# Kernel tuning notes

Measured on AMD Instinct MI355X. Metric: run time of the kernel, lower is better.

The kernel has to match this reference:

```python
import jax, jax.numpy as jnp
import numpy as np

N, D, H, DEG = 20000, 128, 128, 32


def setup_inputs() -> dict:
    key = jax.random.key(0)
    ks = jax.random.split(key, 6)
    s = 0.02
    h = jax.random.normal(ks[0], (N, D), dtype=jnp.float32)
    # per-node neighbor indices, sorted by index (permutation invariance per docstring)
    nbr_idx = jnp.sort(jax.random.randint(ks[1], (N, DEG), 0, N), axis=-1)
    W_ih = jax.random.normal(ks[2], (4 * H, D), dtype=jnp.float32) * s
    W_hh = jax.random.normal(ks[3], (4 * H, H), dtype=jnp.float32) * s
    b_ih = jnp.zeros((4 * H,), jnp.float32)
    b_hh = jnp.zeros((4 * H,), jnp.float32)
    W_out = jax.random.normal(ks[4], (H, D + H), dtype=jnp.float32) * s
    b_out = jnp.zeros((H,), jnp.float32)
    return {"h": h, "nbr_idx": nbr_idx, "W_ih": W_ih, "W_hh": W_hh,
            "b_ih": b_ih, "b_hh": b_hh, "W_out": W_out, "b_out": b_out}


def reference(h, nbr_idx, W_ih, W_hh, b_ih, b_hh, W_out, b_out):
    # Gather neighbor features: [N, DEG, D]
    nbr = h[nbr_idx]
    # Precompute input-to-gate projections for all steps: [N, DEG, 4H]
    xg = jnp.einsum('ndi,gi->ndg', nbr, W_ih) + b_ih + b_hh
    xg = jnp.swapaxes(xg, 0, 1)  # [DEG, N, 4H] for scan over neighbor sequence
    h0 = jnp.zeros((h.shape[0], W_hh.shape[1]), h.dtype)
    c0 = jnp.zeros_like(h0)

    def step(carry, g_t):
        hp, cp = carry
        g = g_t + hp @ W_hh.T            # [N, 4H]
        i, f, gg, o = jnp.split(g, 4, axis=-1)  # PyTorch gate order i,f,g,o
        c = jax.nn.sigmoid(f) * cp + jax.nn.sigmoid(i) * jnp.tanh(gg)
        hn = jax.nn.sigmoid(o) * jnp.tanh(c)
        return (hn, c), None

    (agg, _), _ = jax.lax.scan(step, (h0, c0), xg)  # agg = final hidden state [N, H]
    combined = jnp.concatenate([h, agg], axis=-1)   # [N, D+H]
    return jax.nn.relu(combined @ W_out.T + b_out)  # [N, H]
```

## Files before the change

kernel.cpp:

```cpp
#include <hip/hip_runtime.h>

#define NN 20000
#define DD 128
#define HH 128
#define G4 512
#define DEG 32
#define NPB 32
#define PAIRS 625
#define GRID2 512

typedef __attribute__((ext_vector_type(4))) float f32x4;
typedef __attribute__((ext_vector_type(8))) short s16x8;

#ifndef __has_builtin
#define __has_builtin(x) 0
#endif

__device__ int g_cnt;

static __device__ __forceinline__ float fexp2(float x){
#if __has_builtin(__builtin_amdgcn_exp2f)
  return __builtin_amdgcn_exp2f(x);
#else
  return exp2f(x);
#endif
}
static __device__ __forceinline__ float frcp(float x){
#if __has_builtin(__builtin_amdgcn_rcpf)
  return __builtin_amdgcn_rcpf(x);
#else
  return 1.f/x;
#endif
}

static __device__ __forceinline__ unsigned cvt_pk_bf16(float lo, float hi){
  unsigned r;
  asm("v_cvt_pk_bf16_f32 %0, %1, %2" : "=v"(r) : "v"(lo), "v"(hi));
  return r;
}
static __device__ __forceinline__ s16x8 ld8bf(const float* __restrict__ p){
  f32x4 a = *(const f32x4*)p;
  f32x4 b = *(const f32x4*)(p+4);
  union{unsigned u[4]; s16x8 v;} z;
  z.u[0]=cvt_pk_bf16(a[0],a[1]);
  z.u[1]=cvt_pk_bf16(a[2],a[3]);
  z.u[2]=cvt_pk_bf16(b[0],b[1]);
  z.u[3]=cvt_pk_bf16(b[2],b[3]);
  return z.v;
}
static __device__ __forceinline__ s16x8 ld8bf_s(const float* __restrict__ p, float s){
  f32x4 a = *(const f32x4*)p;
  f32x4 b = *(const f32x4*)(p+4);
  union{unsigned u[4]; s16x8 v;} z;
  z.u[0]=cvt_pk_bf16(a[0]*s,a[1]*s);
  z.u[1]=cvt_pk_bf16(a[2]*s,a[3]*s);
  z.u[2]=cvt_pk_bf16(b[0]*s,b[1]*s);
  z.u[3]=cvt_pk_bf16(b[2]*s,b[3]*s);
  return z.v;
}
static __device__ __forceinline__ float lo16f(unsigned u){
  union{unsigned x; float f;} v; v.x = u << 16; return v.f;
}
static __device__ __forceinline__ float hi16f(unsigned u){
  union{unsigned x; float f;} v; v.x = u & 0xffff0000u; return v.f;
}
#define NLOG2E -1.44269504f
#define TLOG2E  2.88539008f

__global__ __launch_bounds__(512,2) void k_hp(
    const float* __restrict__ h, const float* __restrict__ W_ih,
    const float* __restrict__ b_ih, const float* __restrict__ b_hh,
    unsigned short* __restrict__ Hp)
{
  if(blockIdx.x==0 && threadIdx.x==0) g_cnt = GRID2;
  const int tid=threadIdx.x, w=tid>>6, lane=tid&63, lo=lane&15, hi=lane>>4;
  const float SC[4]={NLOG2E,NLOG2E,TLOG2E,NLOG2E};
  s16x8 A[4][4];
#pragma unroll
  for(int g=0;g<4;++g){
    const float* wr=W_ih+(size_t)(128*g+16*w+lo)*DD+8*hi;
#pragma unroll
    for(int c=0;c<4;++c) A[g][c]=ld8bf_s(wr+32*c, SC[g]);
  }
  f32x4 bb[4];
#pragma unroll
  for(int g=0;g<4;++g){
    const int gcb=128*g+16*w+4*hi;
    bb[g]=(*(const f32x4*)(b_ih+gcb) + *(const f32x4*)(b_hh+gcb))*SC[g];
  }
  const int nchunk = (blockIdx.x < 57) ? 2 : 1;
  for(int cc=0; cc<nchunk; ++cc){
    const int n0 = ((cc? 256+blockIdx.x : blockIdx.x))*64;
    f32x4 acc[4][4];
#pragma unroll
    for(int g=0;g<4;++g)
#pragma unroll
      for(int nt=0;nt<4;++nt) acc[g][nt]=(f32x4)0.f;
#pragma unroll
    for(int c=0;c<4;++c){
      s16x8 B[4];
#pragma unroll
      for(int nt=0;nt<4;++nt){
        int nd=n0+16*nt+lo; if(nd>=NN) nd=NN-1;
        B[nt]=ld8bf(h+(size_t)nd*DD+32*c+8*hi);
      }
#pragma unroll
      for(int g=0;g<4;++g)
#pragma unroll
        for(int nt=0;nt<4;++nt)
          acc[g][nt]=__builtin_amdgcn_mfma_f32_16x16x32_bf16(A[g][c],B[nt],acc[g][nt],0,0,0);
    }
#pragma unroll
    for(int nt=0;nt<4;++nt){
      int nd=n0+16*nt+lo;
      if(nd<NN){
        unsigned short* p = Hp + (size_t)nd*G4 + w*64 + hi*16;
        uint4 q0, q1;
        q0.x=cvt_pk_bf16(acc[0][nt][0]+bb[0][0], acc[0][nt][1]+bb[0][1]);
        q0.y=cvt_pk_bf16(acc[0][nt][2]+bb[0][2], acc[0][nt][3]+bb[0][3]);
        q0.z=cvt_pk_bf16(acc[1][nt][0]+bb[1][0], acc[1][nt][1]+bb[1][1]);
        q0.w=cvt_pk_bf16(acc[1][nt][2]+bb[1][2], acc[1][nt][3]+bb[1][3]);
        q1.x=cvt_pk_bf16(acc[2][nt][0]+bb[2][0], acc[2][nt][1]+bb[2][1]);
        q1.y=cvt_pk_bf16(acc[2][nt][2]+bb[2][2], acc[2][nt][3]+bb[2][3]);
        q1.z=cvt_pk_bf16(acc[3][nt][0]+bb[3][0], acc[3][nt][1]+bb[3][1]);
        q1.w=cvt_pk_bf16(acc[3][nt][2]+bb[3][2], acc[3][nt][3]+bb[3][3]);
        *(uint4*)p = q0;
        *(uint4*)(p+8) = q1;
      }
    }
  }
}

static __device__ __forceinline__ void unpack_acc(const uint4 q[2], f32x4 acc[4]){
  acc[0][0]=lo16f(q[0].x); acc[0][1]=hi16f(q[0].x); acc[0][2]=lo16f(q[0].y); acc[0][3]=hi16f(q[0].y);
  acc[1][0]=lo16f(q[0].z); acc[1][1]=hi16f(q[0].z); acc[1][2]=lo16f(q[0].w); acc[1][3]=hi16f(q[0].w);
  acc[2][0]=lo16f(q[1].x); acc[2][1]=hi16f(q[1].x); acc[2][2]=lo16f(q[1].y); acc[2][3]=hi16f(q[1].y);
  acc[3][0]=lo16f(q[1].z); acc[3][1]=hi16f(q[1].z); acc[3][2]=lo16f(q[1].w); acc[3][3]=hi16f(q[1].w);
}

static __device__ __forceinline__ void cell_update(const f32x4 acc[4], float C[4],
                                                   char* wb, int waddr){
  float hv[4];
#pragma unroll
  for(int r=0;r<4;++r){
    float ei=fexp2(acc[0][r]);
    float ef=fexp2(acc[1][r]);
    float eg=fexp2(acc[2][r]);
    float eo=fexp2(acc[3][r]);
    float itgT=__builtin_fmaf(eg, TLOG2E, -TLOG2E)*frcp((1.f+ei)*(1.f+eg));
    float Cn=__builtin_fmaf(C[r], frcp(1.f+ef), itgT);
    C[r]=Cn;
    float ec=fexp2(Cn);
    hv[r]=(ec-1.f)*frcp((1.f+eo)*(1.f+ec));
  }
  uint2 pk;
  pk.x=cvt_pk_bf16(hv[0],hv[1]);
  pk.y=cvt_pk_bf16(hv[2],hv[3]);
  *(uint2*)(wb + waddr) = pk;
}

__global__ __launch_bounds__(512,2) void k_lstm(
    const float* __restrict__ h, const int* __restrict__ nbr,
    const float* __restrict__ W_hh, const unsigned short* __restrict__ Hp,
    const float* __restrict__ W_out, const float* __restrict__ b_out,
    float* __restrict__ out)
{
  __shared__ unsigned short hpA[16*HH];
  __shared__ unsigned short hpB[16*HH];
  __shared__ int nlds[DEG*NPB];
  __shared__ int spair;
  const int tid=threadIdx.x, w=tid>>6, lane=tid&63, lo=lane&15, hi=lane>>4;
  const int swz=(lo&7)<<4;
  const int woff=w*64+hi*16;
  const int waddr=((lo*256 + 32*w + 8*hi) ^ swz);
  const float SC[4]={NLOG2E,NLOG2E,TLOG2E,NLOG2E};

  s16x8 A[4][4];
#pragma unroll
  for(int g=0;g<4;++g){
    const float* wr=W_hh+(size_t)(128*g+16*w+lo)*HH+8*hi;
#pragma unroll
    for(int c=0;c<4;++c) A[g][c]=ld8bf_s(wr+32*c, SC[g]);
  }

  int pair = blockIdx.x;
  for(;;){
    const int n0 = pair*NPB;
    {
      unsigned* za=(unsigned*)&hpA[0];
      unsigned* zb=(unsigned*)&hpB[0];
      za[tid]=0u; za[tid+512]=0u;
      zb[tid]=0u; zb[tid+512]=0u;
#pragma unroll
      for(int i=0;i<2;++i){
        int idx=tid+512*i;
        nlds[(idx&31)*NPB + (idx>>5)] = nbr[n0*DEG + idx]*G4;
      }
    }
    __syncthreads();

    float cstA[4]={0.f,0.f,0.f,0.f}, cstB[4]={0.f,0.f,0.f,0.f};
    f32x4 accA[4], accB[4];
#pragma unroll
    for(int g=0;g<4;++g) accB[g]=(f32x4)0.f;

    uint4 qAx[2], qAy[2], qBx[2], qBy[2];
    {
      const unsigned short* ga=Hp+(size_t)nlds[lo]+woff;
      const unsigned short* gb=Hp+(size_t)nlds[16+lo]+woff;
      qAx[0]=*(const uint4*)ga; qAx[1]=*(const uint4*)(ga+8);
      qBx[0]=*(const uint4*)gb; qBx[1]=*(const uint4*)(gb+8);
    }

#define INTERVAL_P(QUSE, QLOAD, TLOAD) { \
      { const unsigned short* gp_=Hp+(size_t)nlds[(TLOAD)*NPB+lo]+woff; \
        QLOAD[0]=*(const uint4*)gp_; QLOAD[1]=*(const uint4*)(gp_+8); } \
      s16x8 Ba[4]; \
      const char* ra=(const char*)&hpA[0]; \
      _Pragma("unroll") \
      for(int c=0;c<4;++c) Ba[c]=*(const s16x8*)(ra + (((lo*256 + 64*c + 16*hi)) ^ swz)); \
      cell_update(accB, cstB, (char*)&hpB[0], waddr); \
      unpack_acc(QUSE, accA); \
      _Pragma("unroll") \
      for(int c=0;c<4;++c) \
        _Pragma("unroll") \
        for(int g=0;g<4;++g) \
          accA[g]=__builtin_amdgcn_mfma_f32_16x16x32_bf16(A[g][c],Ba[c],accA[g],0,0,0); \
      asm volatile("s_waitcnt lgkmcnt(0)\n\ts_barrier" ::: "memory"); }

#define INTERVAL_Q(QUSE, QLOAD, TLOAD) { \
      { const unsigned short* gp_=Hp+(size_t)nlds[(TLOAD)*NPB+16+lo]+woff; \
        QLOAD[0]=*(const uint4*)gp_; QLOAD[1]=*(const uint4*)(gp_+8); } \
      s16x8 Bb[4]; \
      const char* rb=(const char*)&hpB[0]; \
      _Pragma("unroll") \
      for(int c=0;c<4;++c) Bb[c]=*(const s16x8*)(rb + (((lo*256 + 64*c + 16*hi)) ^ swz)); \
      cell_update(accA, cstA, (char*)&hpA[0], waddr); \
      unpack_acc(QUSE, accB); \
      _Pragma("unroll") \
      for(int c=0;c<4;++c) \
        _Pragma("unroll") \
        for(int g=0;g<4;++g) \
          accB[g]=__builtin_amdgcn_mfma_f32_16x16x32_bf16(A[g][c],Bb[c],accB[g],0,0,0); \
      asm volatile("s_waitcnt lgkmcnt(0)\n\ts_barrier" ::: "memory"); }

    for(int k=0;k<DEG/2;++k){
      const int t1=2*k+1;
      const int t2 = (t1+1<DEG)? t1+1 : t1;
      INTERVAL_P(qAx, qAy, t1)
      INTERVAL_Q(qBx, qBy, t1)
      INTERVAL_P(qAy, qAx, t2)
      INTERVAL_Q(qBy, qBx, t2)
    }
#undef INTERVAL_P
#undef INTERVAL_Q

    cell_update(accB, cstB, (char*)&hpB[0], waddr);
    asm volatile("s_waitcnt lgkmcnt(0)\n\ts_barrier" ::: "memory");

    s16x8 AO[8];
    {
      const float* wr=W_out+(size_t)(16*w+lo)*256+8*hi;
#pragma unroll
      for(int c=0;c<8;++c) AO[c]=ld8bf(wr+32*c);
    }
    const int ob=16*w+4*hi;
    f32x4 bias=*(const f32x4*)(b_out+ob);
#pragma unroll
    for(int nt=0;nt<2;++nt){
      const int node=n0+nt*16+lo;
      s16x8 BB[8];
      const float* hr=h+(size_t)node*DD+8*hi;
#pragma unroll
      for(int c=0;c<4;++c) BB[c]=ld8bf(hr+32*c);
      const char* rb=(const char*)(nt? &hpB[0] : &hpA[0]);
#pragma unroll
      for(int c=0;c<4;++c)
        BB[4+c]=*(const s16x8*)(rb + (((lo*256 + 64*c + 16*hi)) ^ swz));
      f32x4 acc=(f32x4)0.f;
#pragma unroll
      for(int c=0;c<8;++c) acc=__builtin_amdgcn_mfma_f32_16x16x32_bf16(AO[c],BB[c],acc,0,0,0);
#pragma unroll
      for(int r=0;r<4;++r){ float v=acc[r]+bias[r]; acc[r]=v>0.f?v:0.f; }
      *(f32x4*)(out+(size_t)node*HH+ob)=acc;
    }

    if(tid==0) spair = atomicAdd(&g_cnt, 1);
    __syncthreads();
    pair = spair;
    if(pair >= PAIRS) break;
  }
}

extern "C" void kernel_launch(void* const* d_in, const int* in_sizes, int n_in,
                              void* d_out, int out_size, void* d_ws, size_t ws_size,
                              hipStream_t stream)
{
  const float* h     = (const float*)d_in[0];
  const int*   nbr   = (const int*)d_in[1];
  const float* W_ih  = (const float*)d_in[2];
  const float* W_hh  = (const float*)d_in[3];
  const float* b_ih  = (const float*)d_in[4];
  const float* b_hh  = (const float*)d_in[5];
  const float* W_out = (const float*)d_in[6];
  const float* b_out = (const float*)d_in[7];
  unsigned short* Hp = (unsigned short*)d_ws;

  k_hp<<<256, 512, 0, stream>>>(h, W_ih, b_ih, b_hh, Hp);
  k_lstm<<<GRID2, 512, 0, stream>>>(h, nbr, W_hh, Hp, W_out, b_out, (float*)d_out);
}
```

Measured before the change: 206.3 us.

## Interleave three 16-node groups per block with one barrier per LSTM step

The LSTM kernel now handles 48 nodes per block as three independent 16-node groups. Within each timestep it runs MFMA and cell update for each group back to back, and double-buffers the hidden state in LDS so only one barrier per step is needed instead of two per interval. The persistent atomic work-queue is replaced by a static grid of 417 blocks with bounds clamping for the tail. Occupancy hint drops to 1 block per CU, trading wave-level parallelism for more in-block instruction-level overlap. Latency hiding now rests on intra-block interleaving, and the static grid removes dynamic load balancing.

```diff
diff --git a/kernel.cpp b/kernel.cpp
--- a/kernel.cpp
+++ b/kernel.cpp
@@ -5,9 +5,8 @@
 #define HH 128
 #define G4 512
 #define DEG 32
-#define NPB 32
-#define PAIRS 625
-#define GRID2 512
+#define NPB 48
+#define NBLK 417
 
 typedef __attribute__((ext_vector_type(4))) float f32x4;
 typedef __attribute__((ext_vector_type(8))) short s16x8;
@@ -15,8 +14,6 @@
 #ifndef __has_builtin
 #define __has_builtin(x) 0
 #endif
-
-__device__ int g_cnt;
 
 static __device__ __forceinline__ float fexp2(float x){
 #if __has_builtin(__builtin_amdgcn_exp2f)
@@ -72,7 +69,6 @@
     const float* __restrict__ b_ih, const float* __restrict__ b_hh,
     unsigned short* __restrict__ Hp)
 {
-  if(blockIdx.x==0 && threadIdx.x==0) g_cnt = GRID2;
   const int tid=threadIdx.x, w=tid>>6, lane=tid&63, lo=lane&15, hi=lane>>4;
   const float SC[4]={NLOG2E,NLOG2E,TLOG2E,NLOG2E};
   s16x8 A[4][4];
@@ -159,17 +155,16 @@
   *(uint2*)(wb + waddr) = pk;
 }
 
-__global__ __launch_bounds__(512,2) void k_lstm(
+__global__ __launch_bounds__(512,1) void k_lstm(
     const float* __restrict__ h, const int* __restrict__ nbr,
     const float* __restrict__ W_hh, const unsigned short* __restrict__ Hp,
     const float* __restrict__ W_out, const float* __restrict__ b_out,
     float* __restrict__ out)
 {
-  __shared__ unsigned short hpA[16*HH];
-  __shared__ unsigned short hpB[16*HH];
+  __shared__ unsigned short hpd[3][2][16*HH];
   __shared__ int nlds[DEG*NPB];
-  __shared__ int spair;
   const int tid=threadIdx.x, w=tid>>6, lane=tid&63, lo=lane&15, hi=lane>>4;
+  const int n0=blockIdx.x*NPB;
   const int swz=(lo&7)<<4;
   const int woff=w*64+hi*16;
   const int waddr=((lo*256 + 32*w + 8*hi) ^ swz);
@@ -182,113 +177,81 @@
 #pragma unroll
     for(int c=0;c<4;++c) A[g][c]=ld8bf_s(wr+32*c, SC[g]);
   }
-
-  int pair = blockIdx.x;
-  for(;;){
-    const int n0 = pair*NPB;
-    {
-      unsigned* za=(unsigned*)&hpA[0];
-      unsigned* zb=(unsigned*)&hpB[0];
-      za[tid]=0u; za[tid+512]=0u;
-      zb[tid]=0u; zb[tid+512]=0u;
-#pragma unroll
-      for(int i=0;i<2;++i){
-        int idx=tid+512*i;
-        nlds[(idx&31)*NPB + (idx>>5)] = nbr[n0*DEG + idx]*G4;
-      }
-    }
-    __syncthreads();
-
-    float cstA[4]={0.f,0.f,0.f,0.f}, cstB[4]={0.f,0.f,0.f,0.f};
-    f32x4 accA[4], accB[4];
-#pragma unroll
-    for(int g=0;g<4;++g) accB[g]=(f32x4)0.f;
-
-    uint4 qAx[2], qAy[2], qBx[2], qBy[2];
-    {
-      const unsigned short* ga=Hp+(size_t)nlds[lo]+woff;
-      const unsigned short* gb=Hp+(size_t)nlds[16+lo]+woff;
-      qAx[0]=*(const uint4*)ga; qAx[1]=*(const uint4*)(ga+8);
-      qBx[0]=*(const uint4*)gb; qBx[1]=*(const uint4*)(gb+8);
-    }
-
-#define INTERVAL_P(QUSE, QLOAD, TLOAD) { \
-      { const unsigned short* gp_=Hp+(size_t)nlds[(TLOAD)*NPB+lo]+woff; \
-        QLOAD[0]=*(const uint4*)gp_; QLOAD[1]=*(const uint4*)(gp_+8); } \
-      s16x8 Ba[4]; \
-      const char* ra=(const char*)&hpA[0]; \
+  {
+#pragma unroll
+    for(int g=0;g<3;++g){
+      unsigned* z=(unsigned*)&hpd[g][0][0];
+      z[tid]=0u; z[tid+512]=0u;
+    }
+#pragma unroll
+    for(int i=0;i<3;++i){
+      int idx=tid+512*i;
+      int node=idx>>5;
+      int src=n0+node; if(src>=NN) src=NN-1;
+      nlds[(idx&31)*NPB + node] = nbr[src*DEG + (idx&31)]*G4;
+    }
+  }
+  __syncthreads();
+
+  float cst[3][4]={{0.f,0.f,0.f,0.f},{0.f,0.f,0.f,0.f},{0.f,0.f,0.f,0.f}};
+
+  uint4 qA[2], qB[2], qC[2];
+  {
+    const unsigned short* gp=Hp+(size_t)nlds[lo]+woff;
+    qA[0]=*(const uint4*)gp; qA[1]=*(const uint4*)(gp+8);
+  }
+
+#define PHASE(g, QUSE, QLOAD, LOFF) { \
+    { const unsigned short* gp_=Hp+(size_t)nlds[LOFF]+woff; \
+      QLOAD[0]=*(const uint4*)gp_; QLOAD[1]=*(const uint4*)(gp_+8); } \
+    s16x8 Bg[4]; \
+    const char* rb_=(const char*)&hpd[g][t&1][0]; \
+    _Pragma("unroll") \
+    for(int c=0;c<4;++c) Bg[c]=*(const s16x8*)(rb_ + (((lo*256 + 64*c + 16*hi)) ^ swz)); \
+    f32x4 acc_[4]; \
+    unpack_acc(QUSE, acc_); \
+    _Pragma("unroll") \
+    for(int c=0;c<4;++c) \
       _Pragma("unroll") \
-      for(int c=0;c<4;++c) Ba[c]=*(const s16x8*)(ra + (((lo*256 + 64*c + 16*hi)) ^ swz)); \
-      cell_update(accB, cstB, (char*)&hpB[0], waddr); \
-      unpack_acc(QUSE, accA); \
-      _Pragma("unroll") \
-      for(int c=0;c<4;++c) \
-        _Pragma("unroll") \
-        for(int g=0;g<4;++g) \
-          accA[g]=__builtin_amdgcn_mfma_f32_16x16x32_bf16(A[g][c],Ba[c],accA[g],0,0,0); \
-      asm volatile("s_waitcnt lgkmcnt(0)\n\ts_barrier" ::: "memory"); }
-
-#define INTERVAL_Q(QUSE, QLOAD, TLOAD) { \
-      { const unsigned short* gp_=Hp+(size_t)nlds[(TLOAD)*NPB+16+lo]+woff; \
-        QLOAD[0]=*(const uint4*)gp_; QLOAD[1]=*(const uint4*)(gp_+8); } \
-      s16x8 Bb[4]; \
-      const char* rb=(const char*)&hpB[0]; \
-      _Pragma("unroll") \
-      for(int c=0;c<4;++c) Bb[c]=*(const s16x8*)(rb + (((lo*256 + 64*c + 16*hi)) ^ swz)); \
-      cell_update(accA, cstA, (char*)&hpA[0], waddr); \
-      unpack_acc(QUSE, accB); \
-      _Pragma("unroll") \
-      for(int c=0;c<4;++c) \
-        _Pragma("unroll") \
-        for(int g=0;g<4;++g) \
-          accB[g]=__builtin_amdgcn_mfma_f32_16x16x32_bf16(A[g][c],Bb[c],accB[g],0,0,0); \
-      asm volatile("s_waitcnt lgkmcnt(0)\n\ts_barrier" ::: "memory"); }
-
-    for(int k=0;k<DEG/2;++k){
-      const int t1=2*k+1;
-      const int t2 = (t1+1<DEG)? t1+1 : t1;
-      INTERVAL_P(qAx, qAy, t1)
-      INTERVAL_Q(qBx, qBy, t1)
-      INTERVAL_P(qAy, qAx, t2)
-      INTERVAL_Q(qBy, qBx, t2)
-    }
-#undef INTERVAL_P
-#undef INTERVAL_Q
-
-    cell_update(accB, cstB, (char*)&hpB[0], waddr);
+      for(int gg=0;gg<4;++gg) \
+        acc_[gg]=__builtin_amdgcn_mfma_f32_16x16x32_bf16(A[gg][c],Bg[c],acc_[gg],0,0,0); \
+    cell_update(acc_, cst[g], (char*)&hpd[g][(t+1)&1][0], waddr); }
+
+  for(int t=0;t<DEG;++t){
+    const int tn=(t+1<DEG)? t+1 : t;
+    PHASE(0, qA, qB, t*NPB + 16 + lo)
+    PHASE(1, qB, qC, t*NPB + 32 + lo)
+    PHASE(2, qC, qA, tn*NPB + lo)
     asm volatile("s_waitcnt lgkmcnt(0)\n\ts_barrier" ::: "memory");
-
-    s16x8 AO[8];
-    {
-      const float* wr=W_out+(size_t)(16*w+lo)*256+8*hi;
-#pragma unroll
-      for(int c=0;c<8;++c) AO[c]=ld8bf(wr+32*c);
-    }
-    const int ob=16*w+4*hi;
-    f32x4 bias=*(const f32x4*)(b_out+ob);
-#pragma unroll
-    for(int nt=0;nt<2;++nt){
-      const int node=n0+nt*16+lo;
-      s16x8 BB[8];
-      const float* hr=h+(size_t)node*DD+8*hi;
-#pragma unroll
-      for(int c=0;c<4;++c) BB[c]=ld8bf(hr+32*c);
-      const char* rb=(const char*)(nt? &hpB[0] : &hpA[0]);
-#pragma unroll
-      for(int c=0;c<4;++c)
-        BB[4+c]=*(const s16x8*)(rb + (((lo*256 + 64*c + 16*hi)) ^ swz));
-      f32x4 acc=(f32x4)0.f;
-#pragma unroll
-      for(int c=0;c<8;++c) acc=__builtin_amdgcn_mfma_f32_16x16x32_bf16(AO[c],BB[c],acc,0,0,0);
-#pragma unroll
-      for(int r=0;r<4;++r){ float v=acc[r]+bias[r]; acc[r]=v>0.f?v:0.f; }
-      *(f32x4*)(out+(size_t)node*HH+ob)=acc;
-    }
-
-    if(tid==0) spair = atomicAdd(&g_cnt, 1);
-    __syncthreads();
-    pair = spair;
-    if(pair >= PAIRS) break;
+  }
+#undef PHASE
+
+  s16x8 AO[8];
+  {
+    const float* wr=W_out+(size_t)(16*w+lo)*256+8*hi;
+#pragma unroll
+    for(int c=0;c<8;++c) AO[c]=ld8bf(wr+32*c);
+  }
+  const int ob=16*w+4*hi;
+  f32x4 bias=*(const f32x4*)(b_out+ob);
+#pragma unroll
+  for(int g=0;g<3;++g){
+    const int node=n0+g*16+lo;
+    const int nc = (node<NN)? node : NN-1;
+    s16x8 BB[8];
+    const float* hr=h+(size_t)nc*DD+8*hi;
+#pragma unroll
+    for(int c=0;c<4;++c) BB[c]=ld8bf(hr+32*c);
+    const char* rb=(const char*)&hpd[g][0][0];
+#pragma unroll
+    for(int c=0;c<4;++c)
+      BB[4+c]=*(const s16x8*)(rb + (((lo*256 + 64*c + 16*hi)) ^ swz));
+    f32x4 acc=(f32x4)0.f;
+#pragma unroll
+    for(int c=0;c<8;++c) acc=__builtin_amdgcn_mfma_f32_16x16x32_bf16(AO[c],BB[c],acc,0,0,0);
+#pragma unroll
+    for(int r=0;r<4;++r){ float v=acc[r]+bias[r]; acc[r]=v>0.f?v:0.f; }
+    if(node<NN) *(f32x4*)(out+(size_t)node*HH+ob)=acc;
   }
 }
 
@@ -307,5 +270,5 @@
   unsigned short* Hp = (unsigned short*)d_ws;
 
   k_hp<<<256, 512, 0, stream>>>(h, W_ih, b_ih, b_hh, Hp);
-  k_lstm<<<GRID2, 512, 0, stream>>>(h, nbr, W_hh, Hp, W_out, b_out, (float*)d_out);
-}
+  k_lstm<<<NBLK, 512, 0, stream>>>(h, nbr, W_hh, Hp, W_out, b_out, (float*)d_out);
+}
```

After: 212.0 us. 1.03x slower.
